# Performance work log

Measured on AMD Instinct MI355X. Metric: run time of the kernel, lower is better.

Reference implementation:

```python
import jax, jax.numpy as jnp
import numpy as np

N = 16384
D = 512
VOCAB = 100000
EMB_SCALE = 0.05  # keep dot products ~O(1) so exp() is stable, like trained embeddings


def setup_inputs() -> dict:
    key = jax.random.key(0)
    k1, k2, k3, k4 = jax.random.split(key, 4)
    input_emb = jax.random.normal(k1, (N, D), dtype=jnp.float32) * EMB_SCALE
    target_emb = jax.random.normal(k2, (N, D), dtype=jnp.float32) * EMB_SCALE
    target_ids = jax.random.randint(k3, (N,), 0, VOCAB, dtype=jnp.int64) if jax.config.jax_enable_x64 else jax.random.randint(k3, (N,), 0, VOCAB, dtype=jnp.int32)
    # sampling probabilities in (eps, ~0.5) so 1 - q stays well away from 0
    q_probas = jax.random.uniform(k4, (N,), dtype=jnp.float32, minval=1e-4, maxval=0.5)
    # first half positives, second half negatives (static pattern, matches boolean-mask semantics)
    mask = jnp.arange(N) < (N // 2)
    return {"input_emb": input_emb, "target_emb": target_emb, "target_ids": target_ids,
            "q_probas": q_probas, "mask": mask}


def reference(input_emb, target_emb, target_ids, q_probas, mask):
    # mask is a constant selection pattern -> resolve to static index lists (jit-friendly shapes)
    mask_np = np.asarray(mask)
    pos_idx = np.nonzero(mask_np)[0]
    neg_idx = np.nonzero(~mask_np)[0]

    pos_emb = input_emb[pos_idx]                      # [P, D]
    pos_tgt = target_emb[pos_idx]                     # [P, D]
    neg_tgt = target_emb[neg_idx]                     # [Q, D]

    pos_sim = jnp.einsum('pd,pd->p', pos_emb, pos_tgt)          # [P]
    neg_sim = jnp.einsum('pd,qd->pq', pos_emb, neg_tgt)         # [P, Q]

    # accidental-hit mask: 1 where negative id differs from the positive's true id
    miss = (target_ids[pos_idx][:, None] != target_ids[neg_idx]).astype(jnp.float32)  # [P, Q]
    n_miss = jnp.sum(miss, axis=1, keepdims=True)                # [P, 1]

    # logQ correction: subtract log(n_miss * q_neg / (1 - q_pos))
    log_q = jnp.log(n_miss * q_probas[neg_idx][None, :] / (1.0 - q_probas[pos_idx][:, None]))
    neg_exp = jnp.exp(neg_sim - log_q)                           # [P, Q]
    neg_exp_sum = jnp.einsum('pq,pq->p', miss, neg_exp)          # [P]

    pos_exp = jnp.exp(pos_sim)
    batch_loss = jnp.mean(-pos_sim + jnp.log(pos_exp + neg_exp_sum))
    return batch_loss
```

## Files before the change

### kernel.cpp

```cpp
#include <hip/hip_runtime.h>
#include <hip/hip_bf16.h>

#define NPOS 8192
#define NNEG 8192
#define DIM  512
#define VOCAB 100000

#define FP8_SCALE 64.0f
#define ACC_DESCALE (1.0f / 4096.0f)

typedef float f32x4 __attribute__((ext_vector_type(4)));
typedef long  lng2  __attribute__((ext_vector_type(2)));

__device__ __forceinline__ void async_load16(const void* g, void* l) {
    __builtin_amdgcn_global_load_lds(
        (const __attribute__((address_space(1))) void*)g,
        (__attribute__((address_space(3))) void*)l, 16, 0, 0);
}

__global__ void zero_kernel(int* __restrict__ hist, float* __restrict__ S) {
    const int t = blockIdx.x * 256 + threadIdx.x;
    if (t < VOCAB) hist[t] = 0;
    if (t < NPOS)  S[t] = 0.0f;
}

__global__ void prep_kernel(const float* __restrict__ input_emb,
                            const float* __restrict__ target_emb,
                            const int* __restrict__ ids,
                            const float* __restrict__ q_probas,
                            unsigned char* __restrict__ A8,
                            unsigned char* __restrict__ B8,
                            float* __restrict__ w, float* __restrict__ pos_sim,
                            int* __restrict__ hist) {
    const int r    = (blockIdx.x * blockDim.x + threadIdx.x) >> 6;
    const int lane = threadIdx.x & 63;

    const float4* ain = (const float4*)(input_emb  + (size_t)r * DIM);
    const float4* tin = (const float4*)(target_emb + (size_t)r * DIM);
    const float4* bin = (const float4*)(target_emb + (size_t)(NPOS + r) * DIM);

    float4 a0 = ain[lane * 2], a1 = ain[lane * 2 + 1];
    float4 t0 = tin[lane * 2], t1 = tin[lane * 2 + 1];
    float4 b0 = bin[lane * 2], b1 = bin[lane * 2 + 1];

    int alo = __builtin_amdgcn_cvt_pk_fp8_f32(a0.x * FP8_SCALE, a0.y * FP8_SCALE, 0, false);
    alo     = __builtin_amdgcn_cvt_pk_fp8_f32(a0.z * FP8_SCALE, a0.w * FP8_SCALE, alo, true);
    int ahi = __builtin_amdgcn_cvt_pk_fp8_f32(a1.x * FP8_SCALE, a1.y * FP8_SCALE, 0, false);
    ahi     = __builtin_amdgcn_cvt_pk_fp8_f32(a1.z * FP8_SCALE, a1.w * FP8_SCALE, ahi, true);
    int blo = __builtin_amdgcn_cvt_pk_fp8_f32(b0.x * FP8_SCALE, b0.y * FP8_SCALE, 0, false);
    blo     = __builtin_amdgcn_cvt_pk_fp8_f32(b0.z * FP8_SCALE, b0.w * FP8_SCALE, blo, true);
    int bhi = __builtin_amdgcn_cvt_pk_fp8_f32(b1.x * FP8_SCALE, b1.y * FP8_SCALE, 0, false);
    bhi     = __builtin_amdgcn_cvt_pk_fp8_f32(b1.z * FP8_SCALE, b1.w * FP8_SCALE, bhi, true);

    const int s = lane & 7, wnd = lane >> 3;
    const int phys = wnd * 64 + (s & 3) * 16 + (s >> 2) * 8;
    *(int2*)(A8 + (size_t)r * DIM + phys) = make_int2(alo, ahi);
    *(int2*)(B8 + (size_t)r * DIM + phys) = make_int2(blo, bhi);

    float sum = a0.x * t0.x + a0.y * t0.y + a0.z * t0.z + a0.w * t0.w
              + a1.x * t1.x + a1.y * t1.y + a1.z * t1.z + a1.w * t1.w;
    #pragma unroll
    for (int m = 32; m >= 1; m >>= 1) sum += __shfl_xor(sum, m);

    if (lane == 0) {
        pos_sim[r] = sum;
        w[r] = 1.0f / q_probas[NPOS + r];
        atomicAdd(&hist[ids[NPOS + r]], 1);
    }
}

__global__ __launch_bounds__(256) void gemm_kernel(
        const unsigned char* __restrict__ A8, const unsigned char* __restrict__ B8,
        const int* __restrict__ ids, const float* __restrict__ w,
        float* __restrict__ S) {
    __shared__ __align__(16) unsigned char Atile[128 * 64];
    __shared__ __align__(16) unsigned char Btile[128 * 64];

    const int tid  = threadIdx.x;
    const int lane = tid & 63;
    const int wv   = tid >> 6;
    const int wave_m = (wv & 1) * 64;
    const int wave_n = (wv >> 1) * 64;
    const int quad = lane >> 4;
    const int r16  = lane & 15;
    const int bm = blockIdx.x, bn = blockIdx.y;

    f32x4 acc[4][4] = {};

    const int srow_in = lane >> 2;
    const int sgran   = (lane & 3) ^ ((lane >> 3) & 3);
    const size_t a_base = (size_t)(bm * 128) * DIM;
    const size_t b_base = (size_t)(bn * 128) * DIM;

    for (int k0 = 0; k0 < DIM; k0 += 64) {
        if (k0) __syncthreads();
        #pragma unroll
        for (int cc = 0; cc < 2; ++cc) {
            const int chunk = wv * 2 + cc;
            const int row = chunk * 16 + srow_in;
            async_load16(A8 + a_base + (size_t)row * DIM + k0 + sgran * 16,
                         Atile + chunk * 1024);
            async_load16(B8 + b_base + (size_t)row * DIM + k0 + sgran * 16,
                         Btile + chunk * 1024);
        }
        __syncthreads();

        const int slot = quad ^ ((r16 >> 1) & 3);
        lng2 af[4], bg[4];
        #pragma unroll
        for (int i = 0; i < 4; ++i) {
            const int arow = wave_m + i * 16 + r16;
            af[i] = *(const lng2*)(Atile + arow * 64 + slot * 16);
            const int brow = wave_n + i * 16 + r16;
            bg[i] = *(const lng2*)(Btile + brow * 64 + slot * 16);
        }
        #pragma unroll
        for (int i = 0; i < 4; ++i)
            #pragma unroll
            for (int j = 0; j < 4; ++j)
                acc[i][j] = __builtin_amdgcn_mfma_f32_16x16x32_fp8_fp8(af[i].x, bg[j].x, acc[i][j], 0, 0, 0);
        #pragma unroll
        for (int i = 0; i < 4; ++i)
            #pragma unroll
            for (int j = 0; j < 4; ++j)
                acc[i][j] = __builtin_amdgcn_mfma_f32_16x16x32_fp8_fp8(af[i].y, bg[j].y, acc[i][j], 0, 0, 0);
    }

    int idq[4]; float wq[4];
    #pragma unroll
    for (int j = 0; j < 4; ++j) {
        const int q = bn * 128 + wave_n + j * 16 + r16;
        idq[j] = ids[NPOS + q];
        wq[j]  = w[q];
    }
    #pragma unroll
    for (int i = 0; i < 4; ++i) {
        const int p0 = bm * 128 + wave_m + i * 16 + quad * 4;
        #pragma unroll
        for (int rr = 0; rr < 4; ++rr) {
            const int p = p0 + rr;
            const int idp = ids[p];
            float partial = 0.f;
            #pragma unroll
            for (int j = 0; j < 4; ++j) {
                const float e = __expf(acc[i][j][rr] * ACC_DESCALE) * wq[j];
                partial += (idp != idq[j]) ? e : 0.f;
            }
            partial += __shfl_xor(partial, 1);
            partial += __shfl_xor(partial, 2);
            partial += __shfl_xor(partial, 4);
            partial += __shfl_xor(partial, 8);
            if (r16 == 0) atomicAdd(&S[p], partial);
        }
    }
}

__global__ void final_kernel(const float* __restrict__ pos_sim,
                             const float* __restrict__ S,
                             const int* __restrict__ hist,
                             const int* __restrict__ ids,
                             const float* __restrict__ q_probas,
                             float* __restrict__ out) {
    __shared__ float red[256];
    float local = 0.f;
    for (int p = threadIdx.x; p < NPOS; p += 256) {
        const float ps  = pos_sim[p];
        const float n_miss = (float)(NNEG - hist[ids[p]]);
        const float nes = S[p] * (1.0f - q_probas[p]) / n_miss;
        local += -ps + logf(expf(ps) + nes);
    }
    red[threadIdx.x] = local;
    __syncthreads();
    #pragma unroll
    for (int s = 128; s > 0; s >>= 1) {
        if (threadIdx.x < s) red[threadIdx.x] += red[threadIdx.x + s];
        __syncthreads();
    }
    if (threadIdx.x == 0) out[0] = red[0] / (float)NPOS;
}

extern "C" void kernel_launch(void* const* d_in, const int* in_sizes, int n_in,
                              void* d_out, int out_size, void* d_ws, size_t ws_size,
                              hipStream_t stream) {
    const float* input_emb  = (const float*)d_in[0];
    const float* target_emb = (const float*)d_in[1];
    const int*   target_ids = (const int*)d_in[2];
    const float* q_probas   = (const float*)d_in[3];

    char* ws = (char*)d_ws;
    unsigned char* A8 = (unsigned char*)ws;
    unsigned char* B8 = (unsigned char*)(ws + (size_t)NPOS * DIM);
    float*  S       = (float*)(ws + (size_t)NPOS * DIM * 2);
    float*  w       = S + NPOS;
    float*  pos_sim = w + NPOS;
    int*    hist    = (int*)(pos_sim + NPOS);

    zero_kernel<<<(VOCAB + 255) / 256, 256, 0, stream>>>(hist, S);
    prep_kernel<<<2048, 256, 0, stream>>>(input_emb, target_emb, target_ids,
                                          q_probas, A8, B8, w, pos_sim, hist);
    gemm_kernel<<<dim3(64, 64), 256, 0, stream>>>(A8, B8, target_ids, w, S);
    final_kernel<<<1, 256, 0, stream>>>(pos_sim, S, hist, target_ids, q_probas, (float*)d_out);
}
```

Before: 209.7 us.

## Switch FP8 GEMM to 32x32x64 scaled MFMA and memset zeroing

```diff
diff --git a/kernel.cpp b/kernel.cpp
--- a/kernel.cpp
+++ b/kernel.cpp
@@ -8,20 +8,16 @@
 
 #define FP8_SCALE 64.0f
 #define ACC_DESCALE (1.0f / 4096.0f)
-
-typedef float f32x4 __attribute__((ext_vector_type(4)));
-typedef long  lng2  __attribute__((ext_vector_type(2)));
+#define SCALE_ONE 0x7F7F7F7F
+
+typedef float f32x16 __attribute__((ext_vector_type(16)));
+typedef int   i32x4  __attribute__((ext_vector_type(4)));
+typedef int   i32x8  __attribute__((ext_vector_type(8)));
 
 __device__ __forceinline__ void async_load16(const void* g, void* l) {
     __builtin_amdgcn_global_load_lds(
         (const __attribute__((address_space(1))) void*)g,
         (__attribute__((address_space(3))) void*)l, 16, 0, 0);
-}
-
-__global__ void zero_kernel(int* __restrict__ hist, float* __restrict__ S) {
-    const int t = blockIdx.x * 256 + threadIdx.x;
-    if (t < VOCAB) hist[t] = 0;
-    if (t < NPOS)  S[t] = 0.0f;
 }
 
 __global__ void prep_kernel(const float* __restrict__ input_emb,
@@ -52,10 +48,8 @@
     int bhi = __builtin_amdgcn_cvt_pk_fp8_f32(b1.x * FP8_SCALE, b1.y * FP8_SCALE, 0, false);
     bhi     = __builtin_amdgcn_cvt_pk_fp8_f32(b1.z * FP8_SCALE, b1.w * FP8_SCALE, bhi, true);
 
-    const int s = lane & 7, wnd = lane >> 3;
-    const int phys = wnd * 64 + (s & 3) * 16 + (s >> 2) * 8;
-    *(int2*)(A8 + (size_t)r * DIM + phys) = make_int2(alo, ahi);
-    *(int2*)(B8 + (size_t)r * DIM + phys) = make_int2(blo, bhi);
+    *(int2*)(A8 + (size_t)r * DIM + lane * 8) = make_int2(alo, ahi);
+    *(int2*)(B8 + (size_t)r * DIM + lane * 8) = make_int2(blo, bhi);
 
     float sum = a0.x * t0.x + a0.y * t0.y + a0.z * t0.z + a0.w * t0.w
               + a1.x * t1.x + a1.y * t1.y + a1.z * t1.z + a1.w * t1.w;
@@ -81,16 +75,19 @@
     const int wv   = tid >> 6;
     const int wave_m = (wv & 1) * 64;
     const int wave_n = (wv >> 1) * 64;
-    const int quad = lane >> 4;
-    const int r16  = lane & 15;
+    const int l31  = lane & 31;
+    const int h    = lane >> 5;
     const int bm = blockIdx.x, bn = blockIdx.y;
 
-    f32x4 acc[4][4] = {};
+    f32x16 acc[2][2] = {};
 
     const int srow_in = lane >> 2;
     const int sgran   = (lane & 3) ^ ((lane >> 3) & 3);
     const size_t a_base = (size_t)(bm * 128) * DIM;
     const size_t b_base = (size_t)(bn * 128) * DIM;
+
+    const int swz = (l31 >> 1) & 3;
+    const int slo = (2 * h) ^ swz, shi = (2 * h + 1) ^ swz;
 
     for (int k0 = 0; k0 < DIM; k0 += 64) {
         if (k0) __syncthreads();
@@ -105,52 +102,52 @@
         }
         __syncthreads();
 
-        const int slot = quad ^ ((r16 >> 1) & 3);
-        lng2 af[4], bg[4];
-        #pragma unroll
-        for (int i = 0; i < 4; ++i) {
-            const int arow = wave_m + i * 16 + r16;
-            af[i] = *(const lng2*)(Atile + arow * 64 + slot * 16);
-            const int brow = wave_n + i * 16 + r16;
-            bg[i] = *(const lng2*)(Btile + brow * 64 + slot * 16);
+        i32x8 af[2], bg[2];
+        #pragma unroll
+        for (int t = 0; t < 2; ++t) {
+            const unsigned char* ab = Atile + (wave_m + t * 32 + l31) * 64;
+            i32x4 lo = *(const i32x4*)(ab + slo * 16);
+            i32x4 hi = *(const i32x4*)(ab + shi * 16);
+            af[t] = __builtin_shufflevector(lo, hi, 0, 1, 2, 3, 4, 5, 6, 7);
+            const unsigned char* bb = Btile + (wave_n + t * 32 + l31) * 64;
+            lo = *(const i32x4*)(bb + slo * 16);
+            hi = *(const i32x4*)(bb + shi * 16);
+            bg[t] = __builtin_shufflevector(lo, hi, 0, 1, 2, 3, 4, 5, 6, 7);
         }
         #pragma unroll
-        for (int i = 0; i < 4; ++i)
+        for (int ti = 0; ti < 2; ++ti)
             #pragma unroll
-            for (int j = 0; j < 4; ++j)
-                acc[i][j] = __builtin_amdgcn_mfma_f32_16x16x32_fp8_fp8(af[i].x, bg[j].x, acc[i][j], 0, 0, 0);
-        #pragma unroll
-        for (int i = 0; i < 4; ++i)
-            #pragma unroll
-            for (int j = 0; j < 4; ++j)
-                acc[i][j] = __builtin_amdgcn_mfma_f32_16x16x32_fp8_fp8(af[i].y, bg[j].y, acc[i][j], 0, 0, 0);
-    }
-
-    int idq[4]; float wq[4];
-    #pragma unroll
-    for (int j = 0; j < 4; ++j) {
-        const int q = bn * 128 + wave_n + j * 16 + r16;
-        idq[j] = ids[NPOS + q];
-        wq[j]  = w[q];
-    }
-    #pragma unroll
-    for (int i = 0; i < 4; ++i) {
-        const int p0 = bm * 128 + wave_m + i * 16 + quad * 4;
-        #pragma unroll
-        for (int rr = 0; rr < 4; ++rr) {
-            const int p = p0 + rr;
+            for (int tj = 0; tj < 2; ++tj)
+                acc[ti][tj] = __builtin_amdgcn_mfma_scale_f32_32x32x64_f8f6f4(
+                    af[ti], bg[tj], acc[ti][tj], 0, 0, 0, SCALE_ONE, 0, SCALE_ONE);
+    }
+
+    int idq[2]; float wq[2];
+    #pragma unroll
+    for (int tj = 0; tj < 2; ++tj) {
+        const int q = bn * 128 + wave_n + tj * 32 + l31;
+        idq[tj] = ids[NPOS + q];
+        wq[tj]  = w[q];
+    }
+    #pragma unroll
+    for (int ti = 0; ti < 2; ++ti) {
+        #pragma unroll
+        for (int reg = 0; reg < 16; ++reg) {
+            const int prow = (reg & 3) + 8 * (reg >> 2) + 4 * h;
+            const int p = bm * 128 + wave_m + ti * 32 + prow;
             const int idp = ids[p];
             float partial = 0.f;
             #pragma unroll
-            for (int j = 0; j < 4; ++j) {
-                const float e = __expf(acc[i][j][rr] * ACC_DESCALE) * wq[j];
-                partial += (idp != idq[j]) ? e : 0.f;
+            for (int tj = 0; tj < 2; ++tj) {
+                const float e = __expf(acc[ti][tj][reg] * ACC_DESCALE) * wq[tj];
+                partial += (idp != idq[tj]) ? e : 0.f;
             }
             partial += __shfl_xor(partial, 1);
             partial += __shfl_xor(partial, 2);
             partial += __shfl_xor(partial, 4);
             partial += __shfl_xor(partial, 8);
-            if (r16 == 0) atomicAdd(&S[p], partial);
+            partial += __shfl_xor(partial, 16);
+            if (l31 == 0) atomicAdd(&S[p], partial);
         }
     }
 }
@@ -191,11 +188,11 @@
     unsigned char* A8 = (unsigned char*)ws;
     unsigned char* B8 = (unsigned char*)(ws + (size_t)NPOS * DIM);
     float*  S       = (float*)(ws + (size_t)NPOS * DIM * 2);
-    float*  w       = S + NPOS;
+    int*    hist    = (int*)(S + NPOS);
+    float*  w       = (float*)(hist + VOCAB);
     float*  pos_sim = w + NPOS;
-    int*    hist    = (int*)(pos_sim + NPOS);
-
-    zero_kernel<<<(VOCAB + 255) / 256, 256, 0, stream>>>(hist, S);
+
+    hipMemsetAsync(S, 0, (size_t)(NPOS + VOCAB) * 4, stream);
     prep_kernel<<<2048, 256, 0, stream>>>(input_emb, target_emb, target_ids,
                                           q_probas, A8, B8, w, pos_sim, hist);
     gemm_kernel<<<dim3(64, 64), 256, 0, stream>>>(A8, B8, target_ids, w, S);
```

After: 436.6 us. 108% more time.

## Double-buffer LDS tiles in FP8 GEMM and replace zero kernel with memset

Applied to the files above, without the earlier changes.

```diff
diff --git a/kernel.cpp b/kernel.cpp
--- a/kernel.cpp
+++ b/kernel.cpp
@@ -16,12 +16,6 @@
     __builtin_amdgcn_global_load_lds(
         (const __attribute__((address_space(1))) void*)g,
         (__attribute__((address_space(3))) void*)l, 16, 0, 0);
-}
-
-__global__ void zero_kernel(int* __restrict__ hist, float* __restrict__ S) {
-    const int t = blockIdx.x * 256 + threadIdx.x;
-    if (t < VOCAB) hist[t] = 0;
-    if (t < NPOS)  S[t] = 0.0f;
 }
 
 __global__ void prep_kernel(const float* __restrict__ input_emb,
@@ -73,8 +67,8 @@
         const unsigned char* __restrict__ A8, const unsigned char* __restrict__ B8,
         const int* __restrict__ ids, const float* __restrict__ w,
         float* __restrict__ S) {
-    __shared__ __align__(16) unsigned char Atile[128 * 64];
-    __shared__ __align__(16) unsigned char Btile[128 * 64];
+    __shared__ __align__(16) unsigned char Atile[2][128 * 64];
+    __shared__ __align__(16) unsigned char Btile[2][128 * 64];
 
     const int tid  = threadIdx.x;
     const int lane = tid & 63;
@@ -89,30 +83,39 @@
 
     const int srow_in = lane >> 2;
     const int sgran   = (lane & 3) ^ ((lane >> 3) & 3);
-    const size_t a_base = (size_t)(bm * 128) * DIM;
-    const size_t b_base = (size_t)(bn * 128) * DIM;
-
-    for (int k0 = 0; k0 < DIM; k0 += 64) {
-        if (k0) __syncthreads();
-        #pragma unroll
-        for (int cc = 0; cc < 2; ++cc) {
-            const int chunk = wv * 2 + cc;
-            const int row = chunk * 16 + srow_in;
-            async_load16(A8 + a_base + (size_t)row * DIM + k0 + sgran * 16,
-                         Atile + chunk * 1024);
-            async_load16(B8 + b_base + (size_t)row * DIM + k0 + sgran * 16,
-                         Btile + chunk * 1024);
+    const int row0 = wv * 32 + srow_in;
+    const int row1 = wv * 32 + 16 + srow_in;
+    const size_t goff0 = (size_t)row0 * DIM + sgran * 16;
+    const size_t goff1 = (size_t)row1 * DIM + sgran * 16;
+    const unsigned char* a_src = A8 + (size_t)(bm * 128) * DIM;
+    const unsigned char* b_src = B8 + (size_t)(bn * 128) * DIM;
+    const int ldst0 = (wv * 2) * 1024;
+    const int ldst1 = (wv * 2 + 1) * 1024;
+
+    async_load16(a_src + goff0, Atile[0] + ldst0);
+    async_load16(a_src + goff1, Atile[0] + ldst1);
+    async_load16(b_src + goff0, Btile[0] + ldst0);
+    async_load16(b_src + goff1, Btile[0] + ldst1);
+    __syncthreads();
+
+    const int slot = quad ^ ((r16 >> 1) & 3);
+    for (int it = 0; it < 8; ++it) {
+        const int cur = it & 1;
+        if (it < 7) {
+            const size_t kb = (size_t)(it + 1) * 64;
+            async_load16(a_src + kb + goff0, Atile[cur ^ 1] + ldst0);
+            async_load16(a_src + kb + goff1, Atile[cur ^ 1] + ldst1);
+            async_load16(b_src + kb + goff0, Btile[cur ^ 1] + ldst0);
+            async_load16(b_src + kb + goff1, Btile[cur ^ 1] + ldst1);
         }
-        __syncthreads();
-
-        const int slot = quad ^ ((r16 >> 1) & 3);
+
         lng2 af[4], bg[4];
         #pragma unroll
         for (int i = 0; i < 4; ++i) {
             const int arow = wave_m + i * 16 + r16;
-            af[i] = *(const lng2*)(Atile + arow * 64 + slot * 16);
+            af[i] = *(const lng2*)(Atile[cur] + arow * 64 + slot * 16);
             const int brow = wave_n + i * 16 + r16;
-            bg[i] = *(const lng2*)(Btile + brow * 64 + slot * 16);
+            bg[i] = *(const lng2*)(Btile[cur] + brow * 64 + slot * 16);
         }
         #pragma unroll
         for (int i = 0; i < 4; ++i)
@@ -124,6 +127,8 @@
             #pragma unroll
             for (int j = 0; j < 4; ++j)
                 acc[i][j] = __builtin_amdgcn_mfma_f32_16x16x32_fp8_fp8(af[i].y, bg[j].y, acc[i][j], 0, 0, 0);
+
+        if (it < 7) __syncthreads();
     }
 
     int idq[4]; float wq[4];
@@ -191,11 +196,11 @@
     unsigned char* A8 = (unsigned char*)ws;
     unsigned char* B8 = (unsigned char*)(ws + (size_t)NPOS * DIM);
     float*  S       = (float*)(ws + (size_t)NPOS * DIM * 2);
-    float*  w       = S + NPOS;
+    int*    hist    = (int*)(S + NPOS);
+    float*  w       = (float*)(hist + VOCAB);
     float*  pos_sim = w + NPOS;
-    int*    hist    = (int*)(pos_sim + NPOS);
-
-    zero_kernel<<<(VOCAB + 255) / 256, 256, 0, stream>>>(hist, S);
+
+    hipMemsetAsync(S, 0, (size_t)(NPOS + VOCAB) * 4, stream);
     prep_kernel<<<2048, 256, 0, stream>>>(input_emb, target_emb, target_ids,
                                           q_probas, A8, B8, w, pos_sim, hist);
     gemm_kernel<<<dim3(64, 64), 256, 0, stream>>>(A8, B8, target_ids, w, S);
```

Result: no change. 208.2 us (-0.7%).
